# Optimization experiments

Measured on AMD Instinct MI355X. Metric: run time of the kernel, lower is better.

## Reference

```python
import jax, jax.numpy as jnp
import numpy as np

HQ, HKV, D, RD = 32, 8, 128, 64   # q heads, kv heads, head_dim, rotary_dim
EPS = 1e-6


def _rms_norm(x, w, eps):
    # per-head RMSNorm over last dim (non-gemma: scale by w)
    var = jnp.mean(x * x, axis=-1, keepdims=True)
    return x * jax.lax.rsqrt(var + eps) * w


def _partial_rope(x, c, s, rd):
    # x: [T, H, D]; c/s: [T, rd//2]; NeoX half-split rotation on first rd dims
    x1 = x[..., : rd // 2]
    x2 = x[..., rd // 2 : rd]
    c = c[:, None, :]
    s = s[:, None, :]
    return jnp.concatenate([x1 * c - x2 * s, x2 * c + x1 * s, x[..., rd:]], axis=-1)


def setup_inputs() -> dict:
    key = jax.random.key(0)
    ks = jax.random.split(key, 6)
    B, QL, HID, CACHE = 4, 512, 4096, 512
    T = B * QL
    MAXPOS = 4096
    NPAGES, PS, MP = 256, 16, 64  # total pages, page_size, max pages per seq

    hidden_states = jax.random.normal(ks[0], (T, HID), jnp.float32)
    inv = 1.0 / (10000.0 ** (np.arange(0, RD, 2, dtype=np.float64) / RD))
    ang = np.arange(MAXPOS)[:, None] * inv[None, :]
    cos = jnp.asarray(np.cos(ang), jnp.float32)   # [MAXPOS, RD//2]
    sin = jnp.asarray(np.sin(ang), jnp.float32)
    positions = jnp.tile(CACHE + jnp.arange(QL, dtype=jnp.int32), B)  # [T]
    k_cache = jax.random.normal(ks[1], (NPAGES, PS, HKV, D), jnp.float32)
    v_cache = jax.random.normal(ks[2], (NPAGES, PS, HKV, D), jnp.float32)
    page_table = jnp.arange(B * MP, dtype=jnp.int32).reshape(B, MP)
    cache_seqlens = jnp.full((B,), CACHE, jnp.int32)
    cu_seqlens_q = jnp.arange(B + 1, dtype=jnp.int32) * QL
    qkv_weight = jax.random.normal(ks[3], ((HQ + 2 * HKV) * D, HID), jnp.float32) * 0.02
    o_proj_weight = jax.random.normal(ks[4], (HID, HQ * D), jnp.float32) * 0.02
    q_norm_weight = jnp.ones((D,), jnp.float32)
    k_norm_weight = jnp.ones((D,), jnp.float32)
    return dict(hidden_states=hidden_states, cos=cos, sin=sin, positions=positions,
                k_cache=k_cache, v_cache=v_cache, page_table=page_table,
                cache_seqlens=cache_seqlens, cu_seqlens_q=cu_seqlens_q,
                qkv_weight=qkv_weight, o_proj_weight=o_proj_weight,
                q_norm_weight=q_norm_weight, k_norm_weight=k_norm_weight)


def reference(hidden_states, cos, sin, positions, k_cache, v_cache, page_table,
              cache_seqlens, cu_seqlens_q, qkv_weight, o_proj_weight,
              q_norm_weight, k_norm_weight):
    T = hidden_states.shape[0]
    B = cache_seqlens.shape[0]
    QL = T // B                       # equal-length sequences (extend mode)
    PS = k_cache.shape[1]

    # QKV projection + split
    qkv = hidden_states @ qkv_weight.T
    q, k, v = jnp.split(qkv, [HQ * D, (HQ + HKV) * D], axis=-1)

    # per-head QK RMSNorm (q_norm_weight.shape[0] == head_dim branch)
    q = _rms_norm(q.reshape(T, HQ, D), q_norm_weight, EPS)
    k = _rms_norm(k.reshape(T, HKV, D), k_norm_weight, EPS)
    v = v.reshape(T, HKV, D)

    # partial RoPE
    pc, psn = cos[positions], sin[positions]
    q = _partial_rope(q, pc, psn, RD)
    k = _partial_rope(k, pc, psn, RD)

    # paged KV-cache write: absolute slot = cache_seqlens[b] + j
    pos_abs = cache_seqlens[:, None] + jnp.arange(QL, dtype=jnp.int32)[None, :]  # [B,QL]
    pages = jnp.take_along_axis(page_table, pos_abs // PS, axis=1)
    slots = pos_abs % PS
    k_cache = k_cache.at[pages, slots].set(k.reshape(B, QL, HKV, D))
    v_cache = v_cache.at[pages, slots].set(v.reshape(B, QL, HKV, D))

    # gather per-sequence KV from pages: [B, KV, HKV, D]
    KV = page_table.shape[1] * PS
    keys = k_cache[page_table].reshape(B, KV, HKV, D)
    vals = v_cache[page_table].reshape(B, KV, HKV, D)

    # GQA paged attention with causal mask on absolute positions
    G = HQ // HKV
    qh = q.reshape(B, QL, HKV, G, D)
    scale = 1.0 / np.sqrt(D).astype(np.float32)
    scores = jnp.einsum('bqhgd,bkhd->bhgqk', qh, keys) * scale
    kpos = jnp.arange(KV, dtype=jnp.int32)
    mask = kpos[None, None, :] <= pos_abs[:, :, None]                  # [B,QL,KV]
    scores = jnp.where(mask[:, None, None, :, :], scores, -1e30)
    probs = jax.nn.softmax(scores, axis=-1)
    attn = jnp.einsum('bhgqk,bkhd->bqhgd', probs, vals).reshape(T, HQ * D)

    return attn @ o_proj_weight.T
```

## Files before the change

### kernel.cpp

```cpp
#include <hip/hip_runtime.h>

typedef unsigned int   u32;
typedef unsigned short u16;

typedef float  f32x4  __attribute__((ext_vector_type(4)));
typedef u32    u32x4  __attribute__((ext_vector_type(4)));
typedef u16    u16x4  __attribute__((ext_vector_type(4)));
typedef __bf16 bf16x8 __attribute__((ext_vector_type(8)));

union FragU { u16 us[8]; u32x4 q; bf16x8 v; };

__device__ __forceinline__ u32 f2u(float x){ union{float f;u32 u;}c; c.f=x; return c.u; }
__device__ __forceinline__ float u2f(u32 u){ union{float f;u32 u;}c; c.u=u; return c.f; }
__device__ __forceinline__ u16 bfhi(float x){ u32 u=f2u(x); return (u16)((u + 0x7fffu + ((u>>16)&1u))>>16); }
__device__ __forceinline__ float bff(u16 h){ return u2f(((u32)h)<<16); }
__device__ __forceinline__ u32 cvtpk(float a, float b){
  u32 r;
  asm("v_cvt_pk_bf16_f32 %0, %1, %2" : "=v"(r) : "v"(a), "v"(b));
  return r;
}

__device__ __forceinline__ void gload16(const void* g, void* l){
  __builtin_amdgcn_global_load_lds(
      (const __attribute__((address_space(1))) unsigned int*)g,
      (__attribute__((address_space(3))) unsigned int*)l, 16, 0, 0);
}

__global__ __launch_bounds__(256)
void prep_all(const float* __restrict__ s0, u32* __restrict__ d0, int n0,
              const float* __restrict__ s1, u32* __restrict__ d1, int n1,
              const float* __restrict__ s2, u32* __restrict__ d2, int n2,
              const float* __restrict__ k_cache, const float* __restrict__ v_cache,
              const int* __restrict__ page_table,
              u16* __restrict__ k_all, u16* __restrict__ v_allT)
{
  const int tid = threadIdx.x;
  if (blockIdx.x < 2048){
    const int total = n0 + n1 + n2;
    for (int i = blockIdx.x*256 + tid; i < total; i += 2048*256){
      const float* s; u32* d; int j = i;
      if (j < n0)            { s = s0; d = d0; }
      else if (j < n0 + n1)  { s = s1; d = d1; j -= n0; }
      else                   { s = s2; d = d2; j -= n0 + n1; }
      float4 a = reinterpret_cast<const float4*>(s)[2*j];
      float4 b = reinterpret_cast<const float4*>(s)[2*j+1];
      reinterpret_cast<u32x4*>(d)[j] =
        (u32x4){ cvtpk(a.x,a.y), cvtpk(a.z,a.w), cvtpk(b.x,b.y), cvtpk(b.z,b.w) };
    }
    return;
  }
  __shared__ float tb[32][129];
  const int id = blockIdx.x - 2048;
  const int jt = id & 31, h = (id>>5)&7, b = id>>8;
  const int j0 = jt*32;
  {
    int r = tid>>3, c = tid&7;
    int j = j0 + r;
    int page = page_table[b*64 + (j>>4)];
    int slot = j & 15;
    const float* ks = k_cache + (size_t)((page*16 + slot)*8 + h)*128;
    const float* vs = v_cache + (size_t)((page*16 + slot)*8 + h)*128;
    u16* kd = k_all + ((size_t)(b*8+h)*1024 + j)*128;
    #pragma unroll
    for (int i=0;i<2;i++){
      int d0i = (c + 8*i)*8;
      float4 ka = *reinterpret_cast<const float4*>(ks + d0i);
      float4 kb = *reinterpret_cast<const float4*>(ks + d0i + 4);
      *reinterpret_cast<u32x4*>(kd + d0i) =
        (u32x4){ cvtpk(ka.x,ka.y), cvtpk(ka.z,ka.w), cvtpk(kb.x,kb.y), cvtpk(kb.z,kb.w) };
      float4 va = *reinterpret_cast<const float4*>(vs + d0i);
      float4 vb = *reinterpret_cast<const float4*>(vs + d0i + 4);
      tb[r][d0i+0]=va.x; tb[r][d0i+1]=va.y; tb[r][d0i+2]=va.z; tb[r][d0i+3]=va.w;
      tb[r][d0i+4]=vb.x; tb[r][d0i+5]=vb.y; tb[r][d0i+6]=vb.z; tb[r][d0i+7]=vb.w;
    }
  }
  __syncthreads();
  {
    int dout = tid>>1, jh = tid&1;
    u16* vd = v_allT + ((size_t)(b*8+h)*128 + dout)*1024 + j0 + jh*16;
    #pragma unroll
    for (int i=0;i<2;i++){
      int jb = jh*16 + i*8;
      u32x4 o = { cvtpk(tb[jb+0][dout], tb[jb+1][dout]),
                  cvtpk(tb[jb+2][dout], tb[jb+3][dout]),
                  cvtpk(tb[jb+4][dout], tb[jb+5][dout]),
                  cvtpk(tb[jb+6][dout], tb[jb+7][dout]) };
      *reinterpret_cast<u32x4*>(vd + i*8) = o;
    }
  }
}

__global__ __launch_bounds__(256, 2)
void gemm_pkA2(const u16* __restrict__ A, const u16* __restrict__ B,
               float* __restrict__ C, int M, int N, int K)
{
  extern __shared__ char smem[];
  const int tid  = threadIdx.x;
  const int lane = tid & 63;
  const int w    = tid >> 6;
  const int wm = w >> 1, wn = w & 1;
  const int ln = lane & 15, lg = lane >> 4;

  const int nbm = M >> 7;
  const int nbn = N / 192;
  const int nwg = nbm * nbn;
  const int swz = (blockIdx.x & 7) * (nwg >> 3) + (blockIdx.x >> 3);
  const int bm = swz % nbm, bn = swz / nbm;

  const size_t rb = (size_t)K * 2;
  const int lrow  = lane >> 3;
  const int lslot = (lane & 7) ^ (lrow & 7);
  const char* As0 = (const char*)A + (size_t)(bm*128 + w*8 + lrow)*rb + lslot*16;
  const char* Bs0 = (const char*)B + (size_t)(bn*192 + w*8 + lrow)*rb + lslot*16;

  auto stA = [&](int buf, int t) {
    const char* s = As0 + ((size_t)t << 7);
    char* d = smem + buf*40960 + w*1024;
    gload16(s,           d);
    gload16(s +  32*rb,  d + 4096);
    gload16(s +  64*rb,  d + 8192);
    gload16(s +  96*rb,  d + 12288);
  };
  auto stB = [&](int buf, int t) {
    const char* s = Bs0 + ((size_t)t << 7);
    char* d = smem + buf*40960 + 16384 + w*1024;
    gload16(s,           d);
    gload16(s +  32*rb,  d + 4096);
    gload16(s +  64*rb,  d + 8192);
    gload16(s +  96*rb,  d + 12288);
    gload16(s + 128*rb,  d + 16384);
    gload16(s + 160*rb,  d + 20480);
  };

  f32x4 z = {0.f,0.f,0.f,0.f};
  f32x4 acc[4][6];
  #pragma unroll
  for (int i=0;i<4;i++){
    #pragma unroll
    for (int j=0;j<6;j++) acc[i][j] = z;
  }

  const int nt = K >> 6;
  stA(0, 0); stB(0, 0);
  if (nt > 1) { stB(1, 1);
    asm volatile("s_waitcnt vmcnt(6)" ::: "memory");
  } else {
    asm volatile("s_waitcnt vmcnt(0)" ::: "memory");
  }
  __builtin_amdgcn_s_barrier();
  asm volatile("" ::: "memory");

  const int lx7 = ln & 7;

  for (int t = 0; t < nt; ++t){
    const int cur = t & 1;
    const char* bufc = smem + cur*40960;

    FragU bfr[6][2];
    #pragma unroll
    for (int ni=0; ni<6; ni++){
      const int rofs = 16384 + (wn*96 + ni*16 + ln)*128;
      #pragma unroll
      for (int ks=0; ks<2; ks++)
        bfr[ni][ks].q = *reinterpret_cast<const u32x4*>(bufc + rofs + (((ks*4+lg)^lx7)<<4));
    }
    FragU af[2][2];
    #pragma unroll
    for (int mf=0; mf<2; mf++){
      const int rofs = (wm*64 + mf*16 + ln)*128;
      #pragma unroll
      for (int ks=0; ks<2; ks++)
        af[mf][ks].q = *reinterpret_cast<const u32x4*>(bufc + rofs + (((ks*4+lg)^lx7)<<4));
    }
    if (t+1 < nt) stA(cur^1, t+1);
    __builtin_amdgcn_s_barrier();
    __builtin_amdgcn_s_setprio(1);
    #pragma unroll
    for (int ks=0; ks<2; ks++){
      #pragma unroll
      for (int mf=0; mf<2; mf++){
        #pragma unroll
        for (int ni=0; ni<6; ni++)
          acc[mf][ni] = __builtin_amdgcn_mfma_f32_16x16x32_bf16(af[mf][ks].v, bfr[ni][ks].v, acc[mf][ni], 0,0,0);
      }
    }
    __builtin_amdgcn_s_setprio(0);
    asm volatile("s_waitcnt lgkmcnt(0)" ::: "memory");
    __builtin_amdgcn_s_barrier();

    FragU ag[2][2];
    #pragma unroll
    for (int mf=0; mf<2; mf++){
      const int rofs = (wm*64 + (mf+2)*16 + ln)*128;
      #pragma unroll
      for (int ks=0; ks<2; ks++)
        ag[mf][ks].q = *reinterpret_cast<const u32x4*>(bufc + rofs + (((ks*4+lg)^lx7)<<4));
    }
    if (t+2 < nt) stB(cur, t+2);
    __builtin_amdgcn_s_barrier();
    __builtin_amdgcn_s_setprio(1);
    #pragma unroll
    for (int ks=0; ks<2; ks++){
      #pragma unroll
      for (int mf=0; mf<2; mf++){
        #pragma unroll
        for (int ni=0; ni<6; ni++)
          acc[mf+2][ni] = __builtin_amdgcn_mfma_f32_16x16x32_bf16(ag[mf][ks].v, bfr[ni][ks].v, acc[mf+2][ni], 0,0,0);
      }
    }
    __builtin_amdgcn_s_setprio(0);
    if (t+1 < nt){
      if (t+2 < nt) asm volatile("s_waitcnt vmcnt(6)" ::: "memory");
      else          asm volatile("s_waitcnt vmcnt(0)" ::: "memory");
    }
    __builtin_amdgcn_s_barrier();
    asm volatile("" ::: "memory");
  }

  #pragma unroll
  for (int mi=0; mi<4; mi++){
    #pragma unroll
    for (int ni=0; ni<6; ni++){
      const int row0 = bm*128 + wm*64 + mi*16 + lg*4;
      const int col  = bn*192 + wn*96 + ni*16 + ln;
      #pragma unroll
      for (int r=0; r<4; r++)
        C[(size_t)(row0+r)*N + col] = acc[mi][ni][r];
    }
  }
}

__global__ __launch_bounds__(256, 2)
void gemm_pkB2(const u16* __restrict__ A, const u16* __restrict__ B,
               float* __restrict__ C, int M, int N, int K)
{
  extern __shared__ char smem[];
  const int tid  = threadIdx.x;
  const int lane = tid & 63;
  const int w    = tid >> 6;
  const int wm = w >> 1, wn = w & 1;
  const int ln = lane & 15, lg = lane >> 4;

  const int nbm = M >> 7, nbn = N >> 7;
  const int nwg = nbm * nbn;
  const int swz = (blockIdx.x & 7) * (nwg >> 3) + (blockIdx.x >> 3);
  const int bm = swz % nbm, bn = swz / nbm;

  const size_t rb = (size_t)K * 2;
  const int lrow  = lane >> 3;
  const int lslot = (lane & 7) ^ (lrow & 7);
  const char* As0 = (const char*)A + (size_t)(bm*128 + w*8 + lrow)*rb + lslot*16;
  const char* Bs0 = (const char*)B + (size_t)(bn*128 + w*8 + lrow)*rb + lslot*16;

  auto stA = [&](int buf, int t) {
    const char* s = As0 + ((size_t)t << 7);
    char* d = smem + buf*32768 + w*1024;
    gload16(s,           d);
    gload16(s +  32*rb,  d + 4096);
    gload16(s +  64*rb,  d + 8192);
    gload16(s +  96*rb,  d + 12288);
  };
  auto stB = [&](int buf, int t) {
    const char* s = Bs0 + ((size_t)t << 7);
    char* d = smem + buf*32768 + 16384 + w*1024;
    gload16(s,           d);
    gload16(s +  32*rb,  d + 4096);
    gload16(s +  64*rb,  d + 8192);
    gload16(s +  96*rb,  d + 12288);
  };

  f32x4 z = {0.f,0.f,0.f,0.f};
  f32x4 acc[4][4];
  #pragma unroll
  for (int i=0;i<4;i++){
    #pragma unroll
    for (int j=0;j<4;j++) acc[i][j] = z;
  }

  const int nt = K >> 6;
  stA(0, 0); stB(0, 0);
  if (nt > 1) { stB(1, 1);
    asm volatile("s_waitcnt vmcnt(4)" ::: "memory");
  } else {
    asm volatile("s_waitcnt vmcnt(0)" ::: "memory");
  }
  __builtin_amdgcn_s_barrier();
  asm volatile("" ::: "memory");

  const int lx7 = ln & 7;

  for (int t = 0; t < nt; ++t){
    const int cur = t & 1;
    const char* bufc = smem + cur*32768;

    FragU bfr[4][2];
    #pragma unroll
    for (int ni=0; ni<4; ni++){
      const int rofs = 16384 + (wn*64 + ni*16 + ln)*128;
      #pragma unroll
      for (int ks=0; ks<2; ks++)
        bfr[ni][ks].q = *reinterpret_cast<const u32x4*>(bufc + rofs + (((ks*4+lg)^lx7)<<4));
    }
    FragU af[2][2];
    #pragma unroll
    for (int mf=0; mf<2; mf++){
      const int rofs = (wm*64 + mf*16 + ln)*128;
      #pragma unroll
      for (int ks=0; ks<2; ks++)
        af[mf][ks].q = *reinterpret_cast<const u32x4*>(bufc + rofs + (((ks*4+lg)^lx7)<<4));
    }
    if (t+1 < nt) stA(cur^1, t+1);
    __builtin_amdgcn_s_barrier();
    __builtin_amdgcn_s_setprio(1);
    #pragma unroll
    for (int ks=0; ks<2; ks++){
      #pragma unroll
      for (int mf=0; mf<2; mf++){
        #pragma unroll
        for (int ni=0; ni<4; ni++)
          acc[mf][ni] = __builtin_amdgcn_mfma_f32_16x16x32_bf16(af[mf][ks].v, bfr[ni][ks].v, acc[mf][ni], 0,0,0);
      }
    }
    __builtin_amdgcn_s_setprio(0);
    asm volatile("s_waitcnt lgkmcnt(0)" ::: "memory");
    __builtin_amdgcn_s_barrier();

    FragU ag[2][2];
    #pragma unroll
    for (int mf=0; mf<2; mf++){
      const int rofs = (wm*64 + (mf+2)*16 + ln)*128;
      #pragma unroll
      for (int ks=0; ks<2; ks++)
        ag[mf][ks].q = *reinterpret_cast<const u32x4*>(bufc + rofs + (((ks*4+lg)^lx7)<<4));
    }
    if (t+2 < nt) stB(cur, t+2);
    __builtin_amdgcn_s_barrier();
    __builtin_amdgcn_s_setprio(1);
    #pragma unroll
    for (int ks=0; ks<2; ks++){
      #pragma unroll
      for (int mf=0; mf<2; mf++){
        #pragma unroll
        for (int ni=0; ni<4; ni++)
          acc[mf+2][ni] = __builtin_amdgcn_mfma_f32_16x16x32_bf16(ag[mf][ks].v, bfr[ni][ks].v, acc[mf+2][ni], 0,0,0);
      }
    }
    __builtin_amdgcn_s_setprio(0);
    if (t+1 < nt){
      if (t+2 < nt) asm volatile("s_waitcnt vmcnt(4)" ::: "memory");
      else          asm volatile("s_waitcnt vmcnt(0)" ::: "memory");
    }
    __builtin_amdgcn_s_barrier();
    asm volatile("" ::: "memory");
  }

  #pragma unroll
  for (int mi=0; mi<4; mi++){
    #pragma unroll
    for (int ni=0; ni<4; ni++){
      const int row0 = bm*128 + wm*64 + mi*16 + lg*4;
      const int col  = bn*128 + wn*64 + ni*16 + ln;
      #pragma unroll
      for (int r=0; r<4; r++)
        C[(size_t)(row0+r)*N + col] = acc[mi][ni][r];
    }
  }
}

__global__ __launch_bounds__(256)
void norm_rope_scatter(float* __restrict__ qkv, const float* __restrict__ cosT,
                       const float* __restrict__ sinT, const int* __restrict__ positions,
                       const int* __restrict__ cache_seqlens,
                       const float* __restrict__ qw, const float* __restrict__ kw,
                       u16* __restrict__ k_all, u16* __restrict__ v_allT)
{
  const int t = blockIdx.x;
  const int lane = threadIdx.x & 63;
  const int w = threadIdx.x >> 6;
  const int b = t >> 9;
  const int q = t & 511;
  const int pos  = positions[t];
  const int cpos = cache_seqlens[b] + q;
  for (int it=0; it<12; ++it){
    int h = it*4 + w;
    float* xp = qkv + (size_t)t*6144 + h*128 + 2*lane;
    float2 x = *reinterpret_cast<const float2*>(xp);
    if (h < 40){
      float ss = x.x*x.x + x.y*x.y;
      #pragma unroll
      for (int mk=1; mk<64; mk<<=1) ss += __shfl_xor(ss, mk);
      float var = ss*(1.0f/128.0f) + 1e-6f;
      float rq = rsqrtf(var);
      rq = rq*(1.5f - 0.5f*var*rq*rq);
      const float* wt = (h<32) ? qw : kw;
      x.x *= rq*wt[2*lane]; x.y *= rq*wt[2*lane+1];
      float px = __shfl_xor(x.x, 16);
      float py = __shfl_xor(x.y, 16);
      if (lane < 32){
        int ci = pos*32 + 2*(lane&15);
        float2 cc = *reinterpret_cast<const float2*>(cosT + ci);
        float2 sc = *reinterpret_cast<const float2*>(sinT + ci);
        if (lane < 16){ x.x = x.x*cc.x - px*sc.x; x.y = x.y*cc.y - py*sc.y; }
        else          { x.x = x.x*cc.x + px*sc.x; x.y = x.y*cc.y + py*sc.y; }
      }
    }
    if (h < 32){
      *reinterpret_cast<float2*>(xp) = x;
    } else if (h < 40){
      u16* kp = k_all + ((size_t)(b*8 + (h-32))*1024 + cpos)*128 + 2*lane;
      kp[0] = bfhi(x.x); kp[1] = bfhi(x.y);
    } else {
      u16* vp = v_allT + ((size_t)(b*8 + (h-40))*128 + 2*lane)*1024 + cpos;
      vp[0]    = bfhi(x.x);
      vp[1024] = bfhi(x.y);
    }
  }
}

__global__ __launch_bounds__(512)
void attn_fused8(const float* __restrict__ qkv, const u16* __restrict__ k_all,
                 const u16* __restrict__ v_allT, const int* __restrict__ cache_seqlens,
                 u16* __restrict__ attnO)
{
  extern __shared__ char smem[];
  const int tid = threadIdx.x, lane = tid&63, w = tid>>6;
  const int ln = lane&15, lg = lane>>4;
  const int id = blockIdx.x;
  const int qt = id & 3, g = (id>>2)&3, kvh = (id>>4)&7, b = id>>7;
  const int cs = cache_seqlens[b];
  const int h  = kvh*4 + g;
  const int q0 = qt*128 + w*16;
  const float SCALE = 0.08838834764831845f;
  f32x4 z = {0.f,0.f,0.f,0.f};

  FragU qf[4];
  {
    const float* qp = qkv + (size_t)(b*512 + q0 + ln)*6144 + h*128;
    #pragma unroll
    for (int ks=0; ks<4; ks++){
      int d0 = ks*32 + lg*8;
      float4 a = *reinterpret_cast<const float4*>(qp + d0);
      float4 c = *reinterpret_cast<const float4*>(qp + d0 + 4);
      qf[ks].q = (u32x4){
        cvtpk(a.x*SCALE, a.y*SCALE), cvtpk(a.z*SCALE, a.w*SCALE),
        cvtpk(c.x*SCALE, c.y*SCALE), cvtpk(c.z*SCALE, c.w*SCALE) };
    }
  }
  f32x4 O[8];
  #pragma unroll
  for (int i=0;i<8;i++) O[i] = z;
  float lacc[4] = {0.f,0.f,0.f,0.f};
  const int prow0 = cs + q0 + lg*4;
  const int nt = (cs + qt*128 + 128 + 63) >> 6;
  const char* kbase = (const char*)(k_all  + (size_t)(b*8+kvh)*1024*128);
  const char* vbase = (const char*)(v_allT + (size_t)(b*8+kvh)*128*1024);

  auto stK = [&](int buf, int t){
    #pragma unroll
    for (int i=0;i<2;i++){
      int row = i*32 + w*4 + (lane>>4);
      const char* s = kbase + (size_t)(t*64 + row)*256 + (((lane&15) ^ (row&7))<<4);
      gload16(s, smem + buf*16384 + i*8192 + w*1024);
    }
  };
  auto stV = [&](int buf, int t){
    #pragma unroll
    for (int i=0;i<2;i++){
      int row = i*64 + w*8 + (lane>>3);
      const char* s = vbase + (size_t)row*2048 + (size_t)t*128 + (((lane&7) ^ (row&7))<<4);
      gload16(s, smem + 32768 + buf*16384 + i*8192 + w*1024);
    }
  };

  stK(0, 0); stV(0, 0);
  if (nt > 1){ stK(1, 1); stV(1, 1); }

  for (int tile=0; tile<nt; ++tile){
    const int cur = tile & 1;
    const int kv0 = tile*64;
    if (tile+1 < nt) asm volatile("s_waitcnt vmcnt(4)" ::: "memory");
    else             asm volatile("s_waitcnt vmcnt(0)" ::: "memory");
    __builtin_amdgcn_s_barrier();

    const u16* Kc = (const u16*)(smem + cur*16384);
    f32x4 s[4]; s[0]=z; s[1]=z; s[2]=z; s[3]=z;
    #pragma unroll
    for (int ks=0; ks<4; ks++){
      int so = ((ks*4+lg) ^ (ln&7)) << 3;
      #pragma unroll
      for (int n=0; n<4; n++){
        FragU kf;
        kf.q = *reinterpret_cast<const u32x4*>(&Kc[(n*16+ln)*128 + so]);
        s[n] = __builtin_amdgcn_mfma_f32_16x16x32_bf16(qf[ks].v, kf.v, s[n], 0,0,0);
      }
    }

    float pv[4][4];
    if (kv0 + 63 <= cs + q0){
      #pragma unroll
      for (int n=0;n<4;n++){
        #pragma unroll
        for (int r=0;r<4;r++) pv[n][r] = __expf(s[n][r]);
      }
    } else {
      #pragma unroll
      for (int n=0;n<4;n++){
        #pragma unroll
        for (int r=0;r<4;r++){
          bool ok = (kv0 + n*16 + ln) <= (prow0 + r);
          pv[n][r] = ok ? __expf(s[n][r]) : 0.f;
        }
      }
    }
    #pragma unroll
    for (int r=0;r<4;r++) lacc[r] += (pv[0][r] + pv[1][r]) + (pv[2][r] + pv[3][r]);

    #pragma unroll
    for (int n=0;n<4;n++){
      #pragma unroll
      for (int rp=0; rp<2; rp++){
        u32 hpk = cvtpk(pv[n][rp*2], pv[n][rp*2+1]);
        int col  = n*16 + ln;
        int row0 = lg*4 + rp*2;
        int b0 = w*2048 + row0*128 + ((((col>>3) ^ ((row0>>1)&7)))<<4) + (col&7)*2;
        *(u16*)(smem + 65536 + b0)       = (u16)hpk;
        *(u16*)(smem + 65536 + b0 + 128) = (u16)(hpk >> 16);
      }
    }
    FragU pa[2];
    #pragma unroll
    for (int ks2=0; ks2<2; ks2++)
      pa[ks2].q = *reinterpret_cast<const u32x4*>(
          smem + 65536 + w*2048 + ln*128 + (((ks2*4+lg) ^ ((ln>>1)&7))<<4));

    const char* Vb = smem + 32768 + cur*16384;
    #pragma unroll
    for (int nf=0; nf<8; nf++){
      int dr = nf*16 + ln;
      #pragma unroll
      for (int ks2=0; ks2<2; ks2++){
        FragU vf;
        vf.q = *reinterpret_cast<const u32x4*>(Vb + dr*128 + (((ks2*4+lg) ^ (dr&7))<<4));
        O[nf] = __builtin_amdgcn_mfma_f32_16x16x32_bf16(pa[ks2].v, vf.v, O[nf], 0,0,0);
      }
    }
    asm volatile("s_waitcnt lgkmcnt(0)" ::: "memory");
    __builtin_amdgcn_s_barrier();
    if (tile+2 < nt){ stK(cur, tile+2); stV(cur, tile+2); }
  }

  #pragma unroll
  for (int off=1; off<16; off<<=1){
    #pragma unroll
    for (int r=0;r<4;r++) lacc[r] += __shfl_xor(lacc[r], off);
  }
  float il[4];
  #pragma unroll
  for (int r=0;r<4;r++) il[r] = 1.0f / lacc[r];
  u16* op = attnO + (size_t)(b*512 + q0 + lg*4)*4096 + h*128 + ln;
  #pragma unroll
  for (int nf=0; nf<8; nf++){
    #pragma unroll
    for (int r=0;r<4;r++)
      op[(size_t)r*4096 + nf*16] = bfhi(O[nf][r] * il[r]);
  }
}

extern "C" void kernel_launch(void* const* d_in, const int* in_sizes, int n_in,
                              void* d_out, int out_size, void* d_ws, size_t ws_size,
                              hipStream_t stream) {
  const float* hidden    = (const float*)d_in[0];
  const float* cosT      = (const float*)d_in[1];
  const float* sinT      = (const float*)d_in[2];
  const int*   positions = (const int*)  d_in[3];
  const float* k_cache   = (const float*)d_in[4];
  const float* v_cache   = (const float*)d_in[5];
  const int*   page_tab  = (const int*)  d_in[6];
  const int*   cache_sl  = (const int*)  d_in[7];
  const float* qkv_w     = (const float*)d_in[9];
  const float* o_w       = (const float*)d_in[10];
  const float* qnw       = (const float*)d_in[11];
  const float* knw       = (const float*)d_in[12];
  float* out = (float*)d_out;

  float* qkv   = (float*)d_ws;
  u16* k_all   = (u16*)(qkv + 12582912);
  u16* v_allT  = k_all  + 4194304;
  u16* attnPk  = v_allT + 4194304;
  u16* hidPk   = attnPk + 8388608;
  u16* qkvwPk  = hidPk  + 8388608;
  u16* owPk    = qkvwPk + 25165824;
  (void)in_sizes; (void)n_in; (void)out_size; (void)ws_size;

  (void)hipFuncSetAttribute(reinterpret_cast<const void*>(gemm_pkA2),
                            hipFuncAttributeMaxDynamicSharedMemorySize, 81920);
  (void)hipFuncSetAttribute(reinterpret_cast<const void*>(gemm_pkB2),
                            hipFuncAttributeMaxDynamicSharedMemorySize, 65536);
  (void)hipFuncSetAttribute(reinterpret_cast<const void*>(attn_fused8),
                            hipFuncAttributeMaxDynamicSharedMemorySize, 81920);

  hipLaunchKernelGGL(prep_all, dim3(3072), dim3(256), 0, stream,
                     hidden, (u32*)hidPk, 1048576,
                     qkv_w, (u32*)qkvwPk, 3145728,
                     o_w, (u32*)owPk, 2097152,
                     k_cache, v_cache, page_tab, k_all, v_allT);
  hipLaunchKernelGGL(gemm_pkA2, dim3(512), dim3(256), 81920, stream,
                     hidPk, qkvwPk, qkv, 2048, 6144, 4096);
  hipLaunchKernelGGL(norm_rope_scatter, dim3(2048), dim3(256), 0, stream,
                     qkv, cosT, sinT, positions, cache_sl, qnw, knw, k_all, v_allT);
  hipLaunchKernelGGL(attn_fused8, dim3(512), dim3(512), 81920, stream,
                     qkv, k_all, v_allT, cache_sl, attnPk);
  hipLaunchKernelGGL(gemm_pkB2, dim3(512), dim3(256), 65536, stream,
                     attnPk, owPk, out, 2048, 4096, 4096);
}
```

Before: 306.5 us.

## Fuse Q RMSNorm and RoPE into attention prologue; nontemporal loads in prep

Q-head RMSNorm, weight scaling and partial RoPE move out of the standalone norm/rope kernel and into the attention kernel's Q fragment load, so the separate pass only handles the 16 K/V heads. This removes the read and write-back of the 32 Q heads in fp32 (about 16 MB of round-trip traffic). The attention prologue gains extra shuffles, cos/sin and weight loads, and the Q normalization is recomputed once per block. The prep kernel's fp32 loads also become nontemporal to avoid polluting the cache.

```diff
diff --git a/kernel.cpp b/kernel.cpp
--- a/kernel.cpp
+++ b/kernel.cpp
@@ -13,7 +13,6 @@
 __device__ __forceinline__ u32 f2u(float x){ union{float f;u32 u;}c; c.f=x; return c.u; }
 __device__ __forceinline__ float u2f(u32 u){ union{float f;u32 u;}c; c.u=u; return c.f; }
 __device__ __forceinline__ u16 bfhi(float x){ u32 u=f2u(x); return (u16)((u + 0x7fffu + ((u>>16)&1u))>>16); }
-__device__ __forceinline__ float bff(u16 h){ return u2f(((u32)h)<<16); }
 __device__ __forceinline__ u32 cvtpk(float a, float b){
   u32 r;
   asm("v_cvt_pk_bf16_f32 %0, %1, %2" : "=v"(r) : "v"(a), "v"(b));
@@ -42,8 +41,8 @@
       if (j < n0)            { s = s0; d = d0; }
       else if (j < n0 + n1)  { s = s1; d = d1; j -= n0; }
       else                   { s = s2; d = d2; j -= n0 + n1; }
-      float4 a = reinterpret_cast<const float4*>(s)[2*j];
-      float4 b = reinterpret_cast<const float4*>(s)[2*j+1];
+      f32x4 a = __builtin_nontemporal_load(reinterpret_cast<const f32x4*>(s) + 2*j);
+      f32x4 b = __builtin_nontemporal_load(reinterpret_cast<const f32x4*>(s) + 2*j + 1);
       reinterpret_cast<u32x4*>(d)[j] =
         (u32x4){ cvtpk(a.x,a.y), cvtpk(a.z,a.w), cvtpk(b.x,b.y), cvtpk(b.z,b.w) };
     }
@@ -64,12 +63,12 @@
     #pragma unroll
     for (int i=0;i<2;i++){
       int d0i = (c + 8*i)*8;
-      float4 ka = *reinterpret_cast<const float4*>(ks + d0i);
-      float4 kb = *reinterpret_cast<const float4*>(ks + d0i + 4);
+      f32x4 ka = __builtin_nontemporal_load(reinterpret_cast<const f32x4*>(ks + d0i));
+      f32x4 kb = __builtin_nontemporal_load(reinterpret_cast<const f32x4*>(ks + d0i + 4));
       *reinterpret_cast<u32x4*>(kd + d0i) =
         (u32x4){ cvtpk(ka.x,ka.y), cvtpk(ka.z,ka.w), cvtpk(kb.x,kb.y), cvtpk(kb.z,kb.w) };
-      float4 va = *reinterpret_cast<const float4*>(vs + d0i);
-      float4 vb = *reinterpret_cast<const float4*>(vs + d0i + 4);
+      f32x4 va = __builtin_nontemporal_load(reinterpret_cast<const f32x4*>(vs + d0i));
+      f32x4 vb = __builtin_nontemporal_load(reinterpret_cast<const f32x4*>(vs + d0i + 4));
       tb[r][d0i+0]=va.x; tb[r][d0i+1]=va.y; tb[r][d0i+2]=va.z; tb[r][d0i+3]=va.w;
       tb[r][d0i+4]=vb.x; tb[r][d0i+5]=vb.y; tb[r][d0i+6]=vb.z; tb[r][d0i+7]=vb.w;
     }
@@ -368,11 +367,11 @@
 }
 
 __global__ __launch_bounds__(256)
-void norm_rope_scatter(float* __restrict__ qkv, const float* __restrict__ cosT,
-                       const float* __restrict__ sinT, const int* __restrict__ positions,
-                       const int* __restrict__ cache_seqlens,
-                       const float* __restrict__ qw, const float* __restrict__ kw,
-                       u16* __restrict__ k_all, u16* __restrict__ v_allT)
+void norm_rope_kv(const float* __restrict__ qkv, const float* __restrict__ cosT,
+                  const float* __restrict__ sinT, const int* __restrict__ positions,
+                  const int* __restrict__ cache_seqlens,
+                  const float* __restrict__ kw,
+                  u16* __restrict__ k_all, u16* __restrict__ v_allT)
 {
   const int t = blockIdx.x;
   const int lane = threadIdx.x & 63;
@@ -381,19 +380,18 @@
   const int q = t & 511;
   const int pos  = positions[t];
   const int cpos = cache_seqlens[b] + q;
-  for (int it=0; it<12; ++it){
-    int h = it*4 + w;
-    float* xp = qkv + (size_t)t*6144 + h*128 + 2*lane;
+  for (int it=0; it<4; ++it){
+    int hh = it*4 + w;
+    const float* xp = qkv + (size_t)t*6144 + (32+hh)*128 + 2*lane;
     float2 x = *reinterpret_cast<const float2*>(xp);
-    if (h < 40){
+    if (hh < 8){
       float ss = x.x*x.x + x.y*x.y;
       #pragma unroll
       for (int mk=1; mk<64; mk<<=1) ss += __shfl_xor(ss, mk);
       float var = ss*(1.0f/128.0f) + 1e-6f;
       float rq = rsqrtf(var);
       rq = rq*(1.5f - 0.5f*var*rq*rq);
-      const float* wt = (h<32) ? qw : kw;
-      x.x *= rq*wt[2*lane]; x.y *= rq*wt[2*lane+1];
+      x.x *= rq*kw[2*lane]; x.y *= rq*kw[2*lane+1];
       float px = __shfl_xor(x.x, 16);
       float py = __shfl_xor(x.y, 16);
       if (lane < 32){
@@ -403,14 +401,10 @@
         if (lane < 16){ x.x = x.x*cc.x - px*sc.x; x.y = x.y*cc.y - py*sc.y; }
         else          { x.x = x.x*cc.x + px*sc.x; x.y = x.y*cc.y + py*sc.y; }
       }
-    }
-    if (h < 32){
-      *reinterpret_cast<float2*>(xp) = x;
-    } else if (h < 40){
-      u16* kp = k_all + ((size_t)(b*8 + (h-32))*1024 + cpos)*128 + 2*lane;
+      u16* kp = k_all + ((size_t)(b*8 + hh)*1024 + cpos)*128 + 2*lane;
       kp[0] = bfhi(x.x); kp[1] = bfhi(x.y);
     } else {
-      u16* vp = v_allT + ((size_t)(b*8 + (h-40))*128 + 2*lane)*1024 + cpos;
+      u16* vp = v_allT + ((size_t)(b*8 + (hh-8))*128 + 2*lane)*1024 + cpos;
       vp[0]    = bfhi(x.x);
       vp[1024] = bfhi(x.y);
     }
@@ -418,9 +412,11 @@
 }
 
 __global__ __launch_bounds__(512)
-void attn_fused8(const float* __restrict__ qkv, const u16* __restrict__ k_all,
-                 const u16* __restrict__ v_allT, const int* __restrict__ cache_seqlens,
-                 u16* __restrict__ attnO)
+void attn_fused9(const float* __restrict__ qkv, const float* __restrict__ cosT,
+                 const float* __restrict__ sinT, const int* __restrict__ positions,
+                 const float* __restrict__ qw,
+                 const u16* __restrict__ k_all, const u16* __restrict__ v_allT,
+                 const int* __restrict__ cache_seqlens, u16* __restrict__ attnO)
 {
   extern __shared__ char smem[];
   const int tid = threadIdx.x, lane = tid&63, w = tid>>6;
@@ -435,17 +431,55 @@
 
   FragU qf[4];
   {
-    const float* qp = qkv + (size_t)(b*512 + q0 + ln)*6144 + h*128;
+    const int row = b*512 + q0 + ln;
+    const float* qp = qkv + (size_t)row*6144 + h*128;
+    float xq[4][8];
+    float ss = 0.f;
     #pragma unroll
     for (int ks=0; ks<4; ks++){
       int d0 = ks*32 + lg*8;
-      float4 a = *reinterpret_cast<const float4*>(qp + d0);
-      float4 c = *reinterpret_cast<const float4*>(qp + d0 + 4);
-      qf[ks].q = (u32x4){
-        cvtpk(a.x*SCALE, a.y*SCALE), cvtpk(a.z*SCALE, a.w*SCALE),
-        cvtpk(c.x*SCALE, c.y*SCALE), cvtpk(c.z*SCALE, c.w*SCALE) };
-    }
-  }
+      f32x4 a = *reinterpret_cast<const f32x4*>(qp + d0);
+      f32x4 c = *reinterpret_cast<const f32x4*>(qp + d0 + 4);
+      xq[ks][0]=a.x; xq[ks][1]=a.y; xq[ks][2]=a.z; xq[ks][3]=a.w;
+      xq[ks][4]=c.x; xq[ks][5]=c.y; xq[ks][6]=c.z; xq[ks][7]=c.w;
+      #pragma unroll
+      for (int k2=0;k2<8;k2++) ss += xq[ks][k2]*xq[ks][k2];
+    }
+    ss += __shfl_xor(ss, 16);
+    ss += __shfl_xor(ss, 32);
+    float var = ss*(1.0f/128.0f) + 1e-6f;
+    float rq = rsqrtf(var);
+    rq = rq*(1.5f - 0.5f*var*rq*rq);
+    rq *= SCALE;
+    #pragma unroll
+    for (int ks=0; ks<4; ks++){
+      int d0 = ks*32 + lg*8;
+      f32x4 wa = *reinterpret_cast<const f32x4*>(qw + d0);
+      f32x4 wb = *reinterpret_cast<const f32x4*>(qw + d0 + 4);
+      xq[ks][0]*=rq*wa.x; xq[ks][1]*=rq*wa.y; xq[ks][2]*=rq*wa.z; xq[ks][3]*=rq*wa.w;
+      xq[ks][4]*=rq*wb.x; xq[ks][5]*=rq*wb.y; xq[ks][6]*=rq*wb.z; xq[ks][7]*=rq*wb.w;
+    }
+    const int pos = positions[row];
+    const int ci = pos*32 + lg*8;
+    #pragma unroll
+    for (int k2=0;k2<8;k2+=4){
+      f32x4 cc = *reinterpret_cast<const f32x4*>(cosT + ci + k2);
+      f32x4 sc = *reinterpret_cast<const f32x4*>(sinT + ci + k2);
+      float cA[4] = {cc.x,cc.y,cc.z,cc.w};
+      float sA[4] = {sc.x,sc.y,sc.z,sc.w};
+      #pragma unroll
+      for (int u=0;u<4;u++){
+        float x1 = xq[0][k2+u], x2 = xq[1][k2+u];
+        xq[0][k2+u] = x1*cA[u] - x2*sA[u];
+        xq[1][k2+u] = x2*cA[u] + x1*sA[u];
+      }
+    }
+    #pragma unroll
+    for (int ks=0; ks<4; ks++)
+      qf[ks].q = (u32x4){ cvtpk(xq[ks][0],xq[ks][1]), cvtpk(xq[ks][2],xq[ks][3]),
+                          cvtpk(xq[ks][4],xq[ks][5]), cvtpk(xq[ks][6],xq[ks][7]) };
+  }
+
   f32x4 O[8];
   #pragma unroll
   for (int i=0;i<8;i++) O[i] = z;
@@ -596,7 +630,7 @@
                             hipFuncAttributeMaxDynamicSharedMemorySize, 81920);
   (void)hipFuncSetAttribute(reinterpret_cast<const void*>(gemm_pkB2),
                             hipFuncAttributeMaxDynamicSharedMemorySize, 65536);
-  (void)hipFuncSetAttribute(reinterpret_cast<const void*>(attn_fused8),
+  (void)hipFuncSetAttribute(reinterpret_cast<const void*>(attn_fused9),
                             hipFuncAttributeMaxDynamicSharedMemorySize, 81920);
 
   hipLaunchKernelGGL(prep_all, dim3(3072), dim3(256), 0, stream,
@@ -606,10 +640,10 @@
                      k_cache, v_cache, page_tab, k_all, v_allT);
   hipLaunchKernelGGL(gemm_pkA2, dim3(512), dim3(256), 81920, stream,
                      hidPk, qkvwPk, qkv, 2048, 6144, 4096);
-  hipLaunchKernelGGL(norm_rope_scatter, dim3(2048), dim3(256), 0, stream,
-                     qkv, cosT, sinT, positions, cache_sl, qnw, knw, k_all, v_allT);
-  hipLaunchKernelGGL(attn_fused8, dim3(512), dim3(512), 81920, stream,
-                     qkv, k_all, v_allT, cache_sl, attnPk);
+  hipLaunchKernelGGL(norm_rope_kv, dim3(2048), dim3(256), 0, stream,
+                     qkv, cosT, sinT, positions, cache_sl, knw, k_all, v_allT);
+  hipLaunchKernelGGL(attn_fused9, dim3(512), dim3(512), 81920, stream,
+                     qkv, cosT, sinT, positions, qnw, k_all, v_allT, cache_sl, attnPk);
   hipLaunchKernelGGL(gemm_pkB2, dim3(512), dim3(256), 65536, stream,
                      attnPk, owPk, out, 2048, 4096, 4096);
 }
```

Result: faster. 294.0 us (-4.1%).
